# Kernel tuning notes

Hardware: AMD Instinct MI355X
Metric: run time of the kernel (lower is better)

Reference implementation:

```python
import jax, jax.numpy as jnp
import numpy as np
from jax import lax

GAIN = 16.0           # encoder_gains[0]
TEMP = 0.3            # soft_round_temperature
MASK = 9              # mask_size
PAD = 4               # (MASK - 1) // 2
# dim_arm = 16 causal taps inside the 9x9 mask (all indices < center index 40)
CTX_IDX = [12, 13, 14, 20, 21, 22, 23, 24, 28, 29, 30, 31, 32, 33, 38, 39]
CTX_OFF = [(i // MASK, i % MASK) for i in CTX_IDX]
IMG_H, IMG_W = 1024, 1536
N_GRIDS = 7
SIZES = [(int(np.ceil(IMG_H / 2 ** i)), int(np.ceil(IMG_W / 2 ** i))) for i in range(N_GRIDS)]
N_TOTAL = sum(h * w for h, w in SIZES)  # 2097024


def _softround(x, t):
    fl = jnp.floor(x)
    return fl + 0.5 * jnp.tanh((x - fl - 0.5) / t) / jnp.tanh(0.5 / t) + 0.5


def _forward(latents, noise_u, arm_w1, arm_b1, arm_w2, arm_b2, arm_wo, arm_bo,
             ups_k, pre_k, syn_w1, syn_b1, syn_w2, syn_b2):
    # --- quantize latents: softround(softround(x*g) + kumaraswamy noise), a=1 -> uniform-0.5 ---
    flat = jnp.concatenate([l.reshape(-1) for l in latents]) * GAIN
    flat_q = _softround(_softround(flat, TEMP) + (noise_u - 0.5), TEMP)
    dec, cnt = [], 0
    for h, w in SIZES:
        dec.append(flat_q[cnt:cnt + h * w].reshape(1, 1, h, w))
        cnt += h * w
    # --- _get_neighbor: masked causal context gather (16 taps of the 9x9 mask) ---
    ctxs = []
    for l in dec:
        h, w = l.shape[2], l.shape[3]
        xp = jnp.pad(l[0, 0], PAD)  # zero pad, matches F.pad constant 0
        ctxs.append(jnp.stack([xp[dy:dy + h, dx:dx + w] for dy, dx in CTX_OFF], axis=-1).reshape(-1, len(CTX_OFF)))
    ctx = jnp.concatenate(ctxs, axis=0)  # [N, 16]
    # --- ARM MLP: residual hidden layers, final linear to (mu, log_scale) ---
    h1 = jax.nn.relu(ctx @ arm_w1.T + arm_b1 + ctx)
    h2 = jax.nn.relu(h1 @ arm_w2.T + arm_b2 + h1)
    raw = h2 @ arm_wo.T + arm_bo
    mu, log_s = raw[:, 0], raw[:, 1]
    scale = jnp.exp(-0.5 * jnp.clip(log_s, -13.8155, 13.8155))
    def lcdf(x):
        return 0.5 - 0.5 * jnp.sign(x - mu) * jnp.expm1(-jnp.abs(x - mu) / scale)
    proba = jnp.maximum(lcdf(flat_q + 0.5) - lcdf(flat_q - 0.5), 2.0 ** -16)
    rate = -jnp.log2(proba)
    # --- upsampling: coarse-to-fine, depthwise separable convT x2 + preconcat filter ---
    x = dec[-1]
    for step, i in enumerate(range(N_GRIDS - 1, 0, -1)):
        c = x.shape[1]
        kern = jnp.broadcast_to(jnp.outer(ups_k[step], ups_k[step])[None, None], (c, 1, 8, 8))
        x = lax.conv_general_dilated(x, kern, (1, 1), ((4, 4), (4, 4)), lhs_dilation=(2, 2),
                                     dimension_numbers=('NCHW', 'OIHW', 'NCHW'), feature_group_count=c)
        ht, wt = SIZES[i - 1]
        x = x[:, :, :ht, :wt]
        pk2 = jnp.outer(pre_k[step], pre_k[step])[None, None]  # (1,1,7,7)
        t = lax.conv_general_dilated(dec[i - 1], pk2, (1, 1), ((3, 3), (3, 3)),
                                     dimension_numbers=('NCHW', 'OIHW', 'NCHW'))
        x = jnp.concatenate([t, x], axis=1)
    # --- synthesis: 1x1 conv 7->48 relu, 48->6, split mean / log_scale ---
    hid = jax.nn.relu(jnp.einsum('bchw,oc->bohw', x, syn_w1) + syn_b1[None, :, None, None])
    out = jnp.einsum('bchw,oc->bohw', hid, syn_w2) + syn_b2[None, :, None, None]
    pixel_mean, pixel_log_scale = out[:, :3], out[:, 3:]
    # F.interpolate to img_size is identity here (already full resolution)
    decoded = jnp.clip(pixel_mean, 0.0, 1.0)
    return pixel_mean, pixel_log_scale, decoded, rate


def setup_inputs():
    key = jax.random.key(0)
    ks = jax.random.split(key, 16)
    d = {}
    for i, (h, w) in enumerate(SIZES):
        d['latent%d' % i] = jax.random.uniform(ks[i], (1, 1, h, w), jnp.float32, -0.5, 0.5)
    d['noise_u'] = jax.random.uniform(ks[7], (N_TOTAL,), jnp.float32)
    d['arm_w1'] = jax.random.normal(ks[8], (16, 16), jnp.float32) * 0.25
    d['arm_b1'] = jnp.zeros((16,), jnp.float32)
    d['arm_w2'] = jax.random.normal(ks[9], (16, 16), jnp.float32) * 0.25
    d['arm_b2'] = jnp.zeros((16,), jnp.float32)
    d['arm_wo'] = jax.random.normal(ks[10], (2, 16), jnp.float32) * 0.25
    d['arm_bo'] = jnp.zeros((2,), jnp.float32)
    d['ups_k'] = jax.random.normal(ks[11], (6, 8), jnp.float32) * 0.2 + 0.125
    d['pre_k'] = jax.random.normal(ks[12], (6, 7), jnp.float32) * 0.2 + 0.1
    d['syn_w1'] = jax.random.normal(ks[13], (48, 7), jnp.float32) * 0.3
    d['syn_b1'] = jnp.zeros((48,), jnp.float32)
    d['syn_w2'] = jax.random.normal(ks[14], (6, 48), jnp.float32) * 0.1
    d['syn_b2'] = jnp.zeros((6,), jnp.float32)
    return d


def reference(latent0, latent1, latent2, latent3, latent4, latent5, latent6, noise_u,
              arm_w1, arm_b1, arm_w2, arm_b2, arm_wo, arm_bo,
              ups_k, pre_k, syn_w1, syn_b1, syn_w2, syn_b2):
    return _forward([latent0, latent1, latent2, latent3, latent4, latent5, latent6], noise_u,
                    arm_w1, arm_b1, arm_w2, arm_b2, arm_wo, arm_bo,
                    ups_k, pre_k, syn_w1, syn_b1, syn_w2, syn_b2)
```

## Files before the change

### kernel.cpp

```cpp
#include <hip/hip_runtime.h>
#include <math.h>

#define N_TOTAL 2097024
#define HWF (1024 * 1536)

#define OFF0 0
#define OFF1 1572864
#define OFF2 1966080
#define OFF3 2064384
#define OFF4 2088960
#define OFF5 2095104
#define OFF6 2096640

#define OUT_LS   (3 * HWF)
#define OUT_DEC  (6 * HWF)
#define OUT_RATE (9 * HWF)

typedef float f4 __attribute__((ext_vector_type(4), aligned(4)));
typedef float f2 __attribute__((ext_vector_type(2), aligned(4)));
typedef float f4a16 __attribute__((ext_vector_type(4), aligned(16)));
typedef _Float16 h2 __attribute__((ext_vector_type(2)));
typedef __fp16 fp16v2 __attribute__((ext_vector_type(2)));

__device__ __forceinline__ h2 as_h2(unsigned u) {
    union { unsigned u; h2 h; } x; x.u = u; return x.h;
}
__device__ __forceinline__ h2 pkrtz(float a, float b) {
    union { fp16v2 f; h2 h; } x;
    x.f = __builtin_amdgcn_cvt_pkrtz(a, b);
    return x.h;
}
__device__ __forceinline__ float dot2f(h2 a, h2 b, float c) {
#if __has_builtin(__builtin_amdgcn_fdot2)
    return __builtin_amdgcn_fdot2(a, b, c, false);
#else
    return fmaf((float)a[0], (float)b[0], fmaf((float)a[1], (float)b[1], c));
#endif
}

__device__ __forceinline__ float softround_f(float x) {
    const float INV_T = 1.0f / 0.3f;
    const float HALF_OVER_TANH = 0.53699381f;
    float fl = floorf(x);
    float z = (x - fl - 0.5f) * INV_T;
    float e = __expf(2.0f * z);
    float th = 1.0f - 2.0f * __builtin_amdgcn_rcpf(e + 1.0f);
    return fl + th * HALF_OVER_TANH + 0.5f;
}

__global__ void pack_weights_kernel(const float* __restrict__ w1, const float* __restrict__ b1,
                                    const float* __restrict__ w2, unsigned* __restrict__ wp) {
    int t = threadIdx.x;
    if (t < 192) {
        int k = t >> 2, p = t & 3;
        float x = w1[k * 7 + 2 * p];
        float y = (p < 3) ? w1[k * 7 + 2 * p + 1] : b1[k];
        union { h2 h; unsigned u; } c;
        c.h = (h2){(_Float16)x, (_Float16)y};
        wp[t] = c.u;
    } else if (t < 336) {
        int r = t - 192;
        int o = r / 24, kk = r - o * 24;
        union { h2 h; unsigned u; } c;
        c.h = (h2){(_Float16)w2[o * 48 + 2 * kk], (_Float16)w2[o * 48 + 2 * kk + 1]};
        wp[t] = c.u;
    }
}

__global__ void quant_kernel(const float* __restrict__ l0, const float* __restrict__ l1,
                             const float* __restrict__ l2, const float* __restrict__ l3,
                             const float* __restrict__ l4, const float* __restrict__ l5,
                             const float* __restrict__ l6, const float* __restrict__ noise,
                             float* __restrict__ flat_q) {
    int idx = (blockIdx.x * 256 + threadIdx.x) * 4;
    if (idx >= N_TOTAL) return;
    const float* src;
    int base;
    if      (idx < OFF1) { src = l0; base = idx - OFF0; }
    else if (idx < OFF2) { src = l1; base = idx - OFF1; }
    else if (idx < OFF3) { src = l2; base = idx - OFF2; }
    else if (idx < OFF4) { src = l3; base = idx - OFF3; }
    else if (idx < OFF5) { src = l4; base = idx - OFF4; }
    else if (idx < OFF6) { src = l5; base = idx - OFF5; }
    else                 { src = l6; base = idx - OFF6; }
    f4a16 v = *(const f4a16*)(src + base);
    f4a16 n = *(const f4a16*)(noise + idx);
    f4a16 r;
#pragma unroll
    for (int c = 0; c < 4; c++) {
        float x = v[c] * 16.0f;
        float s1 = softround_f(x);
        r[c] = softround_f(s1 + n[c] - 0.5f);
    }
    *(f4a16*)(flat_q + idx) = r;
}

template <int H, int W, int OFFT>
__device__ __forceinline__ void arm_body(const float* __restrict__ flat_q, int pos,
                                         const float* __restrict__ w1, const float* __restrict__ b1,
                                         const float* __restrict__ w2, const float* __restrict__ b2,
                                         const float* __restrict__ wo, const float* __restrict__ bo,
                                         float* __restrict__ rate_out) {
    if (pos >= H * W) return;
    unsigned up = (unsigned)pos;
    int y = up / (unsigned)W;
    int x = pos - y * W;
    const float* g = flat_q + OFFT + (size_t)y * W + x;

    float ctx[16];
    if (y >= 3 && x >= 3 && x <= W - 3) {
        f4 r3  = *(const f4*)(g - 3 * W - 1);
        f4 r2a = *(const f4*)(g - 2 * W - 2);
        float r2b = g[-2 * W + 2];
        f4 r1a = *(const f4*)(g - W - 3);
        f2 r1b = *(const f2*)(g - W + 1);
        f2 r0  = *(const f2*)(g - 2);
        ctx[0] = r3.x;  ctx[1] = r3.y;  ctx[2] = r3.z;
        ctx[3] = r2a.x; ctx[4] = r2a.y; ctx[5] = r2a.z; ctx[6] = r2a.w; ctx[7] = r2b;
        ctx[8] = r1a.x; ctx[9] = r1a.y; ctx[10] = r1a.z; ctx[11] = r1a.w;
        ctx[12] = r1b.x; ctx[13] = r1b.y;
        ctx[14] = r0.x; ctx[15] = r0.y;
    } else {
        const int DY[16] = {-3,-3,-3,-2,-2,-2,-2,-2,-1,-1,-1,-1,-1,-1, 0, 0};
        const int DX[16] = {-1, 0, 1,-2,-1, 0, 1, 2,-3,-2,-1, 0, 1, 2,-2,-1};
#pragma unroll
        for (int k = 0; k < 16; k++) {
            int yy = y + DY[k], xx = x + DX[k];
            ctx[k] = (yy >= 0 && yy < H && xx >= 0 && xx < W)
                         ? flat_q[OFFT + (size_t)yy * W + xx] : 0.0f;
        }
    }

    float h1[16];
#pragma unroll 4
    for (int j = 0; j < 16; j++) {
        float acc = b1[j] + ctx[j];
#pragma unroll
        for (int k = 0; k < 16; k++) acc = fmaf(w1[j * 16 + k], ctx[k], acc);
        h1[j] = fmaxf(acc, 0.0f);
    }
    float h2v[16];
#pragma unroll 4
    for (int j = 0; j < 16; j++) {
        float acc = b2[j] + h1[j];
#pragma unroll
        for (int k = 0; k < 16; k++) acc = fmaf(w2[j * 16 + k], h1[k], acc);
        h2v[j] = fmaxf(acc, 0.0f);
    }
    float mu = bo[0], ls = bo[1];
#pragma unroll
    for (int k = 0; k < 16; k++) {
        mu = fmaf(wo[k], h2v[k], mu);
        ls = fmaf(wo[16 + k], h2v[k], ls);
    }
    ls = fminf(fmaxf(ls, -13.8155f), 13.8155f);
    float inv_scale = __expf(0.5f * ls);

    float q = g[0];
    float da = (q + 0.5f) - mu;
    float db = (q - 0.5f) - mu;
    float ea = __expf(-fabsf(da) * inv_scale);
    float eb = __expf(-fabsf(db) * inv_scale);
    float la = 0.5f - 0.5f * copysignf(1.0f, da) * (ea - 1.0f);
    float lb = 0.5f - 0.5f * copysignf(1.0f, db) * (eb - 1.0f);
    float proba = fmaxf(la - lb, 1.52587890625e-05f);
    rate_out[OFFT + pos] = -__log2f(proba);
}

__global__ __launch_bounds__(256) void arm_all_kernel(
    const float* __restrict__ flat_q,
    const float* __restrict__ w1, const float* __restrict__ b1,
    const float* __restrict__ w2, const float* __restrict__ b2,
    const float* __restrict__ wo, const float* __restrict__ bo,
    float* __restrict__ rate_out) {
    int b = blockIdx.x;
    int t = threadIdx.x;
    if (b < 6144) {
        arm_body<1024, 1536, OFF0>(flat_q, b * 256 + t, w1, b1, w2, b2, wo, bo, rate_out);
    } else if (b < 7680) {
        arm_body<512, 768, OFF1>(flat_q, (b - 6144) * 256 + t, w1, b1, w2, b2, wo, bo, rate_out);
    } else if (b < 8064) {
        arm_body<256, 384, OFF2>(flat_q, (b - 7680) * 256 + t, w1, b1, w2, b2, wo, bo, rate_out);
    } else if (b < 8160) {
        arm_body<128, 192, OFF3>(flat_q, (b - 8064) * 256 + t, w1, b1, w2, b2, wo, bo, rate_out);
    } else if (b < 8184) {
        arm_body<64, 96, OFF4>(flat_q, (b - 8160) * 256 + t, w1, b1, w2, b2, wo, bo, rate_out);
    } else if (b < 8190) {
        arm_body<32, 48, OFF5>(flat_q, (b - 8184) * 256 + t, w1, b1, w2, b2, wo, bo, rate_out);
    } else {
        arm_body<16, 24, OFF6>(flat_q, (b - 8190) * 256 + t, w1, b1, w2, b2, wo, bo, rate_out);
    }
}

__device__ __forceinline__ void up_quad(const float* __restrict__ in, int H, int W,
                                        int i, int j, const float* K, float o[4]) {
    float w[5][5];
    bool interior = (i >= 2 && i <= H - 3 && j >= 2 && j <= W - 3);
    if (interior) {
        const float* p = in + (i - 2) * W + (j - 2);
#pragma unroll
        for (int r = 0; r < 5; r++) {
            f4 a = *(const f4*)p;
            w[r][0] = a.x; w[r][1] = a.y; w[r][2] = a.z; w[r][3] = a.w;
            w[r][4] = p[4];
            p += W;
        }
    } else {
#pragma unroll
        for (int r = 0; r < 5; r++)
#pragma unroll
            for (int e = 0; e < 5; e++) {
                int yy = i - 2 + r, xx = j - 2 + e;
                w[r][e] = (yy >= 0 && yy < H && xx >= 0 && xx < W) ? in[yy * W + xx] : 0.0f;
            }
    }
    float h0[5], h1[5];
#pragma unroll
    for (int r = 0; r < 5; r++) {
        h0[r] = K[0]*w[r][0] + K[2]*w[r][1] + K[4]*w[r][2] + K[6]*w[r][3];
        h1[r] = K[1]*w[r][1] + K[3]*w[r][2] + K[5]*w[r][3] + K[7]*w[r][4];
    }
    o[0] = K[0]*h0[0] + K[2]*h0[1] + K[4]*h0[2] + K[6]*h0[3];
    o[1] = K[0]*h1[0] + K[2]*h1[1] + K[4]*h1[2] + K[6]*h1[3];
    o[2] = K[1]*h0[1] + K[3]*h0[2] + K[5]*h0[3] + K[7]*h0[4];
    o[3] = K[1]*h1[1] + K[3]*h1[2] + K[5]*h1[3] + K[7]*h1[4];
}

__device__ __forceinline__ void conv7_quad(const float* __restrict__ dec, int H, int W,
                                           int i, int j, const float* k, float o[4]) {
    int Y = 2 * i, X = 2 * j;
    float g0[8], g1[8];
    bool interior = (Y - 3 >= 0 && Y + 4 <= H - 1 && X - 3 >= 0 && X + 4 <= W - 1);
    if (interior) {
        const float* p = dec + (Y - 3) * W + (X - 3);
#pragma unroll
        for (int r = 0; r < 8; r++) {
            f4 a = *(const f4*)p;
            f4 b = *(const f4*)(p + 4);
            g0[r] = k[0]*a.x + k[1]*a.y + k[2]*a.z + k[3]*a.w + k[4]*b.x + k[5]*b.y + k[6]*b.z;
            g1[r] = k[0]*a.y + k[1]*a.z + k[2]*a.w + k[3]*b.x + k[4]*b.y + k[5]*b.z + k[6]*b.w;
            p += W;
        }
    } else {
#pragma unroll
        for (int r = 0; r < 8; r++) {
            float wv[8];
#pragma unroll
            for (int q = 0; q < 8; q++) {
                int yy = Y - 3 + r, xx = X - 3 + q;
                wv[q] = (yy >= 0 && yy < H && xx >= 0 && xx < W) ? dec[yy * W + xx] : 0.0f;
            }
            g0[r] = k[0]*wv[0] + k[1]*wv[1] + k[2]*wv[2] + k[3]*wv[3] + k[4]*wv[4] + k[5]*wv[5] + k[6]*wv[6];
            g1[r] = k[0]*wv[1] + k[1]*wv[2] + k[2]*wv[3] + k[3]*wv[4] + k[4]*wv[5] + k[5]*wv[6] + k[6]*wv[7];
        }
    }
    o[0] = k[0]*g0[0] + k[1]*g0[1] + k[2]*g0[2] + k[3]*g0[3] + k[4]*g0[4] + k[5]*g0[5] + k[6]*g0[6];
    o[1] = k[0]*g1[0] + k[1]*g1[1] + k[2]*g1[2] + k[3]*g1[3] + k[4]*g1[4] + k[5]*g1[5] + k[6]*g1[6];
    o[2] = k[0]*g0[1] + k[1]*g0[2] + k[2]*g0[3] + k[3]*g0[4] + k[4]*g0[5] + k[5]*g0[6] + k[6]*g0[7];
    o[3] = k[0]*g1[1] + k[1]*g1[2] + k[2]*g1[3] + k[3]*g1[4] + k[4]*g1[5] + k[5]*g1[6] + k[6]*g1[7];
}

__global__ void pyramid_quad_kernel(const float* __restrict__ xin, int hin, int win_,
                                    const float* __restrict__ dec,
                                    const float* __restrict__ upsk, const float* __restrict__ prek,
                                    float* __restrict__ xout, int hout, int wout) {
    int qw = wout >> 1, qh = hout >> 1;
    int j = blockIdx.x * blockDim.x + threadIdx.x;
    int i = blockIdx.y * blockDim.y + threadIdx.y;
    int c = blockIdx.z;
    if (j >= qw || i >= qh) return;
    float o[4];
    if (c == 0) {
        float k[7];
#pragma unroll
        for (int p = 0; p < 7; p++) k[p] = prek[p];
        conv7_quad(dec, hout, wout, i, j, k, o);
    } else {
        float K[8];
#pragma unroll
        for (int p = 0; p < 8; p++) K[p] = upsk[p];
        up_quad(xin + (size_t)(c - 1) * hin * win_, hin, win_, i, j, K, o);
    }
    size_t base = ((size_t)c * hout + 2 * i) * wout + 2 * j;
    *(float2*)(xout + base)        = make_float2(o[0], o[1]);
    *(float2*)(xout + base + wout) = make_float2(o[2], o[3]);
}

__global__ __launch_bounds__(256) void final_kernel(
    const float* __restrict__ up_in,
    const float* __restrict__ dec0,
    const float* __restrict__ upsk, const float* __restrict__ prek,
    const unsigned* __restrict__ wp,
    const float* __restrict__ b2,
    float* __restrict__ out) {
    const int H2_ = 512, W2_ = 768, H1_ = 1024, W1_ = 1536;
    int t = threadIdx.x;
    int X  = blockIdx.x * 64 + (t & 63);
    int ip = blockIdx.y * 4 + (t >> 6);
    int Y = 2 * ip;

    float K[8], kp[7];
#pragma unroll
    for (int p = 0; p < 8; p++) K[p] = upsk[p];
#pragma unroll
    for (int p = 0; p < 7; p++) kp[p] = prek[p];

    float pxe[7], pxo[7];

    {
        float g[8];
        bool interior = (Y >= 4 && Y <= H1_ - 6 && X >= 3 && X <= W1_ - 5);
        if (interior) {
            const float* p = dec0 + (size_t)(Y - 3) * W1_ + (X - 3);
#pragma unroll
            for (int r = 0; r < 8; r++) {
                f4 a = *(const f4*)p;
                f4 b = *(const f4*)(p + 4);
                g[r] = kp[0]*a.x + kp[1]*a.y + kp[2]*a.z + kp[3]*a.w
                     + kp[4]*b.x + kp[5]*b.y + kp[6]*b.z;
                p += W1_;
            }
        } else {
#pragma unroll
            for (int r = 0; r < 8; r++) {
                float s = 0.0f;
#pragma unroll
                for (int q = 0; q < 7; q++) {
                    int yy = Y - 3 + r, xx = X - 3 + q;
                    float v = (yy >= 0 && yy < H1_ && xx >= 0 && xx < W1_)
                                  ? dec0[(size_t)yy * W1_ + xx] : 0.0f;
                    s = fmaf(kp[q], v, s);
                }
                g[r] = s;
            }
        }
        float oe = 0.0f, oo = 0.0f;
#pragma unroll
        for (int r = 0; r < 7; r++) {
            oe = fmaf(kp[r], g[r], oe);
            oo = fmaf(kp[r], g[r + 1], oo);
        }
        pxe[0] = oe; pxo[0] = oo;
    }

    {
        int q0 = X & 1;
        int j0 = (X >> 1) - 2 + q0;
        float kh[4], kv0[4], kv1[4];
#pragma unroll
        for (int e = 0; e < 4; e++) {
            kh[e]  = K[2 * e + q0];
            kv0[e] = K[2 * e];
            kv1[e] = K[2 * e + 1];
        }
        bool interior = (ip >= 2 && ip <= H2_ - 3 && j0 >= 0 && j0 + 3 < W2_);
#pragma unroll
        for (int c = 0; c < 6; c++) {
            const float* base = up_in + (size_t)c * (H2_ * W2_);
            float h[5];
            if (interior) {
                const float* p = base + (size_t)(ip - 2) * W2_ + j0;
#pragma unroll
                for (int r = 0; r < 5; r++) {
                    f4 a = *(const f4*)p;
                    h[r] = kh[0]*a.x + kh[1]*a.y + kh[2]*a.z + kh[3]*a.w;
                    p += W2_;
                }
            } else {
#pragma unroll
                for (int r = 0; r < 5; r++) {
                    float s = 0.0f;
#pragma unroll
                    for (int e = 0; e < 4; e++) {
                        int yy = ip - 2 + r, xx = j0 + e;
                        float v = (yy >= 0 && yy < H2_ && xx >= 0 && xx < W2_)
                                      ? base[(size_t)yy * W2_ + xx] : 0.0f;
                        s = fmaf(kh[e], v, s);
                    }
                    h[r] = s;
                }
            }
            pxe[c + 1] = kv0[0]*h[0] + kv0[1]*h[1] + kv0[2]*h[2] + kv0[3]*h[3];
            pxo[c + 1] = kv1[0]*h[1] + kv1[1]*h[2] + kv1[2]*h[3] + kv1[3]*h[4];
        }
    }

    h2 ppe[4], ppo[4];
#pragma unroll
    for (int c = 0; c < 3; c++) {
        ppe[c] = pkrtz(pxe[2 * c], pxe[2 * c + 1]);
        ppo[c] = pkrtz(pxo[2 * c], pxo[2 * c + 1]);
    }
    ppe[3] = pkrtz(pxe[6], 1.0f);
    ppo[3] = pkrtz(pxo[6], 1.0f);

    float acce[6], acco[6];
#pragma unroll
    for (int o = 0; o < 6; o++) { acce[o] = b2[o]; acco[o] = b2[o]; }
    const unsigned* w1p = wp;
    const unsigned* w2p = wp + 192;
#pragma unroll 4
    for (int kk = 0; kk < 24; kk++) {
        h2 wk0[4], wk1[4];
#pragma unroll
        for (int p = 0; p < 4; p++) {
            wk0[p] = as_h2(w1p[(2 * kk) * 4 + p]);
            wk1[p] = as_h2(w1p[(2 * kk + 1) * 4 + p]);
        }
        float s0e = 0.0f, s1e = 0.0f, s0o = 0.0f, s1o = 0.0f;
#pragma unroll
        for (int p = 0; p < 4; p++) {
            s0e = dot2f(wk0[p], ppe[p], s0e);
            s1e = dot2f(wk1[p], ppe[p], s1e);
            s0o = dot2f(wk0[p], ppo[p], s0o);
            s1o = dot2f(wk1[p], ppo[p], s1o);
        }
        h2 hpe = pkrtz(fmaxf(s0e, 0.0f), fmaxf(s1e, 0.0f));
        h2 hpo = pkrtz(fmaxf(s0o, 0.0f), fmaxf(s1o, 0.0f));
#pragma unroll
        for (int o = 0; o < 6; o++) {
            h2 w2k = as_h2(w2p[o * 24 + kk]);
            acce[o] = dot2f(w2k, hpe, acce[o]);
            acco[o] = dot2f(w2k, hpo, acco[o]);
        }
    }

    size_t pe = (size_t)Y * W1_ + X;
    size_t po = pe + W1_;
#pragma unroll
    for (int c = 0; c < 3; c++) {
        out[(size_t)c * HWF + pe] = acce[c];
        out[(size_t)c * HWF + po] = acco[c];
        out[OUT_LS + (size_t)c * HWF + pe] = acce[c + 3];
        out[OUT_LS + (size_t)c * HWF + po] = acco[c + 3];
        out[OUT_DEC + (size_t)c * HWF + pe] = fminf(fmaxf(acce[c], 0.0f), 1.0f);
        out[OUT_DEC + (size_t)c * HWF + po] = fminf(fmaxf(acco[c], 0.0f), 1.0f);
    }
}

extern "C" void kernel_launch(void* const* d_in, const int* in_sizes, int n_in,
                              void* d_out, int out_size, void* d_ws, size_t ws_size,
                              hipStream_t stream) {
    const float* lat[7];
    for (int i = 0; i < 7; i++) lat[i] = (const float*)d_in[i];
    const float* noise  = (const float*)d_in[7];
    const float* arm_w1 = (const float*)d_in[8];
    const float* arm_b1 = (const float*)d_in[9];
    const float* arm_w2 = (const float*)d_in[10];
    const float* arm_b2 = (const float*)d_in[11];
    const float* arm_wo = (const float*)d_in[12];
    const float* arm_bo = (const float*)d_in[13];
    const float* ups_k  = (const float*)d_in[14];
    const float* pre_k  = (const float*)d_in[15];
    const float* syn_w1 = (const float*)d_in[16];
    const float* syn_b1 = (const float*)d_in[17];
    const float* syn_w2 = (const float*)d_in[18];
    const float* syn_b2 = (const float*)d_in[19];
    float* out = (float*)d_out;

    float* flat_q = (float*)d_ws;
    float* bufA   = flat_q + N_TOTAL;
    float* bufB   = bufA + 6 * 512 * 768;
    unsigned* wpack = (unsigned*)(bufB + 5 * 256 * 384);

    static const int SH[7]  = {1024, 512, 256, 128, 64, 32, 16};
    static const int SW[7]  = {1536, 768, 384, 192, 96, 48, 24};
    static const int OFF[7] = {OFF0, OFF1, OFF2, OFF3, OFF4, OFF5, OFF6};

    pack_weights_kernel<<<1, 512, 0, stream>>>(syn_w1, syn_b1, syn_w2, wpack);

    quant_kernel<<<(N_TOTAL / 4 + 255) / 256, 256, 0, stream>>>(
        lat[0], lat[1], lat[2], lat[3], lat[4], lat[5], lat[6], noise, flat_q);

    arm_all_kernel<<<8192, 256, 0, stream>>>(flat_q, arm_w1, arm_b1, arm_w2, arm_b2,
                                             arm_wo, arm_bo, out + OUT_RATE);

    const float* xin = flat_q + OFF6;
    float* bufs[2] = {bufA, bufB};
    for (int s = 0; s < 5; s++) {
        int i    = 6 - s;
        int hin  = SH[i], win_ = SW[i];
        int hout = SH[i - 1], wout = SW[i - 1];
        float* xout = bufs[s & 1];
        dim3 blk(16, 16);
        dim3 grd((wout / 2 + 15) / 16, (hout / 2 + 15) / 16, s + 2);
        pyramid_quad_kernel<<<grd, blk, 0, stream>>>(xin, hin, win_,
                                                     flat_q + OFF[i - 1],
                                                     ups_k + s * 8, pre_k + s * 7,
                                                     xout, hout, wout);
        xin = xout;
    }

    dim3 fgrd(1536 / 64, 512 / 4);
    final_kernel<<<fgrd, 256, 0, stream>>>(bufA, flat_q,
                                           ups_k + 5 * 8, pre_k + 5 * 7,
                                           wpack, syn_b2, out);
}
```

Before: 139.7 us.

## Fuse weight packing into quant kernel and merge coarse pyramid levels into one block

Folds the synthesis-weight packing into the first block of the quantization kernel, which removes one launch. Replaces the three smallest upsampling pyramid steps with a single 1024-thread kernel that keeps the coarsest intermediate in shared memory and syncs between levels. The aim is to cut launch overhead and tail latency from tiny grids. The cost is that one block now does the 128x192 level serially, and that block may be slower than the separate multi-block launches it replaces.

```diff
diff --git a/kernel.cpp b/kernel.cpp
--- a/kernel.cpp
+++ b/kernel.cpp
@@ -48,31 +48,31 @@
     return fl + th * HALF_OVER_TANH + 0.5f;
 }
 
-__global__ void pack_weights_kernel(const float* __restrict__ w1, const float* __restrict__ b1,
-                                    const float* __restrict__ w2, unsigned* __restrict__ wp) {
+__global__ void quant_pack_kernel(const float* __restrict__ l0, const float* __restrict__ l1,
+                                  const float* __restrict__ l2, const float* __restrict__ l3,
+                                  const float* __restrict__ l4, const float* __restrict__ l5,
+                                  const float* __restrict__ l6, const float* __restrict__ noise,
+                                  float* __restrict__ flat_q,
+                                  const float* __restrict__ sw1, const float* __restrict__ sb1,
+                                  const float* __restrict__ sw2, unsigned* __restrict__ wp) {
     int t = threadIdx.x;
-    if (t < 192) {
-        int k = t >> 2, p = t & 3;
-        float x = w1[k * 7 + 2 * p];
-        float y = (p < 3) ? w1[k * 7 + 2 * p + 1] : b1[k];
-        union { h2 h; unsigned u; } c;
-        c.h = (h2){(_Float16)x, (_Float16)y};
-        wp[t] = c.u;
-    } else if (t < 336) {
-        int r = t - 192;
-        int o = r / 24, kk = r - o * 24;
-        union { h2 h; unsigned u; } c;
-        c.h = (h2){(_Float16)w2[o * 48 + 2 * kk], (_Float16)w2[o * 48 + 2 * kk + 1]};
-        wp[t] = c.u;
-    }
-}
-
-__global__ void quant_kernel(const float* __restrict__ l0, const float* __restrict__ l1,
-                             const float* __restrict__ l2, const float* __restrict__ l3,
-                             const float* __restrict__ l4, const float* __restrict__ l5,
-                             const float* __restrict__ l6, const float* __restrict__ noise,
-                             float* __restrict__ flat_q) {
-    int idx = (blockIdx.x * 256 + threadIdx.x) * 4;
+    if (blockIdx.x == 0) {
+        for (int i = t; i < 336; i += 256) {
+            union { h2 h; unsigned u; } c;
+            if (i < 192) {
+                int k = i >> 2, p = i & 3;
+                float x = sw1[k * 7 + 2 * p];
+                float y = (p < 3) ? sw1[k * 7 + 2 * p + 1] : sb1[k];
+                c.h = (h2){(_Float16)x, (_Float16)y};
+            } else {
+                int r = i - 192;
+                int o = r / 24, kk = r - o * 24;
+                c.h = (h2){(_Float16)sw2[o * 48 + 2 * kk], (_Float16)sw2[o * 48 + 2 * kk + 1]};
+            }
+            wp[i] = c.u;
+        }
+    }
+    int idx = (blockIdx.x * 256 + t) * 4;
     if (idx >= N_TOTAL) return;
     const float* src;
     int base;
@@ -93,6 +93,44 @@
         r[c] = softround_f(s1 + n[c] - 0.5f);
     }
     *(f4a16*)(flat_q + idx) = r;
+}
+
+__device__ __forceinline__ float arm_mlp_rate(const float ctx[16], float q,
+                                              const float* __restrict__ w1, const float* __restrict__ b1,
+                                              const float* __restrict__ w2, const float* __restrict__ b2,
+                                              const float* __restrict__ wo, const float* __restrict__ bo) {
+    float h1[16];
+#pragma unroll 4
+    for (int j = 0; j < 16; j++) {
+        float acc = b1[j] + ctx[j];
+#pragma unroll
+        for (int k = 0; k < 16; k++) acc = fmaf(w1[j * 16 + k], ctx[k], acc);
+        h1[j] = fmaxf(acc, 0.0f);
+    }
+    float h2v[16];
+#pragma unroll 4
+    for (int j = 0; j < 16; j++) {
+        float acc = b2[j] + h1[j];
+#pragma unroll
+        for (int k = 0; k < 16; k++) acc = fmaf(w2[j * 16 + k], h1[k], acc);
+        h2v[j] = fmaxf(acc, 0.0f);
+    }
+    float mu = bo[0], ls = bo[1];
+#pragma unroll
+    for (int k = 0; k < 16; k++) {
+        mu = fmaf(wo[k], h2v[k], mu);
+        ls = fmaf(wo[16 + k], h2v[k], ls);
+    }
+    ls = fminf(fmaxf(ls, -13.8155f), 13.8155f);
+    float inv_scale = __expf(0.5f * ls);
+    float da = (q + 0.5f) - mu;
+    float db = (q - 0.5f) - mu;
+    float ea = __expf(-fabsf(da) * inv_scale);
+    float eb = __expf(-fabsf(db) * inv_scale);
+    float la = 0.5f - 0.5f * copysignf(1.0f, da) * (ea - 1.0f);
+    float lb = 0.5f - 0.5f * copysignf(1.0f, db) * (eb - 1.0f);
+    float proba = fmaxf(la - lb, 1.52587890625e-05f);
+    return -__log2f(proba);
 }
 
 template <int H, int W, int OFFT>
@@ -130,41 +168,7 @@
                          ? flat_q[OFFT + (size_t)yy * W + xx] : 0.0f;
         }
     }
-
-    float h1[16];
-#pragma unroll 4
-    for (int j = 0; j < 16; j++) {
-        float acc = b1[j] + ctx[j];
-#pragma unroll
-        for (int k = 0; k < 16; k++) acc = fmaf(w1[j * 16 + k], ctx[k], acc);
-        h1[j] = fmaxf(acc, 0.0f);
-    }
-    float h2v[16];
-#pragma unroll 4
-    for (int j = 0; j < 16; j++) {
-        float acc = b2[j] + h1[j];
-#pragma unroll
-        for (int k = 0; k < 16; k++) acc = fmaf(w2[j * 16 + k], h1[k], acc);
-        h2v[j] = fmaxf(acc, 0.0f);
-    }
-    float mu = bo[0], ls = bo[1];
-#pragma unroll
-    for (int k = 0; k < 16; k++) {
-        mu = fmaf(wo[k], h2v[k], mu);
-        ls = fmaf(wo[16 + k], h2v[k], ls);
-    }
-    ls = fminf(fmaxf(ls, -13.8155f), 13.8155f);
-    float inv_scale = __expf(0.5f * ls);
-
-    float q = g[0];
-    float da = (q + 0.5f) - mu;
-    float db = (q - 0.5f) - mu;
-    float ea = __expf(-fabsf(da) * inv_scale);
-    float eb = __expf(-fabsf(db) * inv_scale);
-    float la = 0.5f - 0.5f * copysignf(1.0f, da) * (ea - 1.0f);
-    float lb = 0.5f - 0.5f * copysignf(1.0f, db) * (eb - 1.0f);
-    float proba = fmaxf(la - lb, 1.52587890625e-05f);
-    rate_out[OFFT + pos] = -__log2f(proba);
+    rate_out[OFFT + pos] = arm_mlp_rate(ctx, g[0], w1, b1, w2, b2, wo, bo);
 }
 
 __global__ __launch_bounds__(256) void arm_all_kernel(
@@ -260,6 +264,79 @@
     o[3] = k[0]*g1[1] + k[1]*g1[2] + k[2]*g1[3] + k[3]*g1[4] + k[4]*g1[5] + k[5]*g1[6] + k[6]*g1[7];
 }
 
+__global__ __launch_bounds__(1024) void pyr012_kernel(
+    const float* __restrict__ flat_q,
+    const float* __restrict__ ups_k, const float* __restrict__ pre_k,
+    float* __restrict__ s1out, float* __restrict__ s2out) {
+    __shared__ float s0[2 * 32 * 48];
+    int t = threadIdx.x;
+
+    if (t < 768) {
+        int c = t / 384;
+        int r = t - c * 384;
+        int i = r / 24, j = r - i * 24;
+        float o[4];
+        if (c == 0) {
+            float k[7];
+#pragma unroll
+            for (int p = 0; p < 7; p++) k[p] = pre_k[p];
+            conv7_quad(flat_q + OFF5, 32, 48, i, j, k, o);
+        } else {
+            float K[8];
+#pragma unroll
+            for (int p = 0; p < 8; p++) K[p] = ups_k[p];
+            up_quad(flat_q + OFF6, 16, 24, i, j, K, o);
+        }
+        int base = (c * 32 + 2 * i) * 48 + 2 * j;
+        s0[base] = o[0]; s0[base + 1] = o[1];
+        s0[base + 48] = o[2]; s0[base + 49] = o[3];
+    }
+    __syncthreads();
+
+    for (int idx = t; idx < 3 * 32 * 48; idx += 1024) {
+        int c = idx / (32 * 48);
+        int r = idx - c * (32 * 48);
+        int i = r / 48, j = r - i * 48;
+        float o[4];
+        if (c == 0) {
+            float k[7];
+#pragma unroll
+            for (int p = 0; p < 7; p++) k[p] = pre_k[7 + p];
+            conv7_quad(flat_q + OFF4, 64, 96, i, j, k, o);
+        } else {
+            float K[8];
+#pragma unroll
+            for (int p = 0; p < 8; p++) K[p] = ups_k[8 + p];
+            up_quad(s0 + (c - 1) * (32 * 48), 32, 48, i, j, K, o);
+        }
+        size_t base = ((size_t)c * 64 + 2 * i) * 96 + 2 * j;
+        s1out[base] = o[0]; s1out[base + 1] = o[1];
+        s1out[base + 96] = o[2]; s1out[base + 97] = o[3];
+    }
+    __syncthreads();
+
+    for (int idx = t; idx < 4 * 64 * 96; idx += 1024) {
+        int c = idx / (64 * 96);
+        int r = idx - c * (64 * 96);
+        int i = r / 96, j = r - i * 96;
+        float o[4];
+        if (c == 0) {
+            float k[7];
+#pragma unroll
+            for (int p = 0; p < 7; p++) k[p] = pre_k[14 + p];
+            conv7_quad(flat_q + OFF3, 128, 192, i, j, k, o);
+        } else {
+            float K[8];
+#pragma unroll
+            for (int p = 0; p < 8; p++) K[p] = ups_k[16 + p];
+            up_quad(s1out + (size_t)(c - 1) * (64 * 96), 64, 96, i, j, K, o);
+        }
+        size_t base = ((size_t)c * 128 + 2 * i) * 192 + 2 * j;
+        s2out[base] = o[0]; s2out[base + 1] = o[1];
+        s2out[base + 192] = o[2]; s2out[base + 193] = o[3];
+    }
+}
+
 __global__ void pyramid_quad_kernel(const float* __restrict__ xin, int hin, int win_,
                                     const float* __restrict__ dec,
                                     const float* __restrict__ upsk, const float* __restrict__ prek,
@@ -461,34 +538,34 @@
     float* flat_q = (float*)d_ws;
     float* bufA   = flat_q + N_TOTAL;
     float* bufB   = bufA + 6 * 512 * 768;
-    unsigned* wpack = (unsigned*)(bufB + 5 * 256 * 384);
-
-    static const int SH[7]  = {1024, 512, 256, 128, 64, 32, 16};
-    static const int SW[7]  = {1536, 768, 384, 192, 96, 48, 24};
-    static const int OFF[7] = {OFF0, OFF1, OFF2, OFF3, OFF4, OFF5, OFF6};
-
-    pack_weights_kernel<<<1, 512, 0, stream>>>(syn_w1, syn_b1, syn_w2, wpack);
-
-    quant_kernel<<<(N_TOTAL / 4 + 255) / 256, 256, 0, stream>>>(
-        lat[0], lat[1], lat[2], lat[3], lat[4], lat[5], lat[6], noise, flat_q);
+    float* s1tmp  = bufB + 5 * 256 * 384;
+    float* s2out  = s1tmp + 3 * 64 * 96;
+    unsigned* wpack = (unsigned*)(s2out + 4 * 128 * 192);
+
+    quant_pack_kernel<<<(N_TOTAL / 4 + 255) / 256, 256, 0, stream>>>(
+        lat[0], lat[1], lat[2], lat[3], lat[4], lat[5], lat[6], noise, flat_q,
+        syn_w1, syn_b1, syn_w2, wpack);
 
     arm_all_kernel<<<8192, 256, 0, stream>>>(flat_q, arm_w1, arm_b1, arm_w2, arm_b2,
                                              arm_wo, arm_bo, out + OUT_RATE);
 
-    const float* xin = flat_q + OFF6;
-    float* bufs[2] = {bufA, bufB};
-    for (int s = 0; s < 5; s++) {
-        int i    = 6 - s;
-        int hin  = SH[i], win_ = SW[i];
-        int hout = SH[i - 1], wout = SW[i - 1];
-        float* xout = bufs[s & 1];
+    pyr012_kernel<<<1, 1024, 0, stream>>>(flat_q, ups_k, pre_k, s1tmp, s2out);
+
+    {
         dim3 blk(16, 16);
-        dim3 grd((wout / 2 + 15) / 16, (hout / 2 + 15) / 16, s + 2);
-        pyramid_quad_kernel<<<grd, blk, 0, stream>>>(xin, hin, win_,
-                                                     flat_q + OFF[i - 1],
-                                                     ups_k + s * 8, pre_k + s * 7,
-                                                     xout, hout, wout);
-        xin = xout;
+        dim3 grd((192 + 15) / 16, (128 + 15) / 16, 5);
+        pyramid_quad_kernel<<<grd, blk, 0, stream>>>(s2out, 128, 192,
+                                                     flat_q + OFF2,
+                                                     ups_k + 3 * 8, pre_k + 3 * 7,
+                                                     bufB, 256, 384);
+    }
+    {
+        dim3 blk(16, 16);
+        dim3 grd((384 + 15) / 16, (256 + 15) / 16, 6);
+        pyramid_quad_kernel<<<grd, blk, 0, stream>>>(bufB, 256, 384,
+                                                     flat_q + OFF1,
+                                                     ups_k + 4 * 8, pre_k + 4 * 7,
+                                                     bufA, 512, 768);
     }
 
     dim3 fgrd(1536 / 64, 512 / 4);
```

Measured after the change: 214.4 us. 53.5% more time.
